# Kernel optimization log

Measured on AMD Instinct MI355X. Metric: run time of the kernel, lower is better.

Reference implementation:

```python
import jax, jax.numpy as jnp
import numpy as np

# PEPS grid configuration (matches init_kwargs)
X, Y = 4, 4            # xnodes, ynodes
D = 6                  # bond_dim
P = 2                  # features_in (physical dim)
F = 10                 # features_out (forced by result.view([10]))
CX, CY = X // 2, Y // 2  # center node carries the output leg
BATCH = 2048


def node_labels(i, j):
    # bond labels after the physical index is contracted away; axis order: up, left, down, right, out
    labs = []
    if i > 0: labs.append(f'v{i-1}_{j}')   # up bond (shared with row i-1)
    if j > 0: labs.append(f'h{i}_{j-1}')   # left bond (shared with col j-1)
    if i < X - 1: labs.append(f'v{i}_{j}') # down bond
    if j < Y - 1: labs.append(f'h{i}_{j}') # right bond
    if (i, j) == (CX, CY): labs.append('o')  # output leg on center node
    return labs


def node_shape(i, j):
    shp = [P]  # physical axis first (input_nodes[i][j][0] ^ peps_nodes[i][j][0])
    shp += [D] * (int(i > 0) + int(j > 0) + int(i < X - 1) + int(j < Y - 1))
    if (i, j) == (CX, CY): shp.append(F)
    return tuple(shp)


def setup_inputs() -> dict:
    key = jax.random.key(0)
    keys = jax.random.split(key, X * Y + 1)
    inp = {"x": jax.random.normal(keys[0], (BATCH, X, Y, P), dtype=jnp.float32)}
    k = 1
    for i in range(X):
        for j in range(Y):
            # simple_peps uniform init with std=0.01
            inp[f"w{i}{j}"] = jax.random.uniform(keys[k], node_shape(i, j), dtype=jnp.float32, minval=-0.01, maxval=0.01)
            k += 1
    return inp


def _td(a, alabs, b, blabs):
    """Label-tracked tensordot over all shared bond labels."""
    shared = [l for l in alabs if l in blabs]
    ai = [alabs.index(l) for l in shared]
    bi = [blabs.index(l) for l in shared]
    out = jnp.tensordot(a, b, axes=(ai, bi))
    labs = [l for l in alabs if l not in shared] + [l for l in blabs if l not in shared]
    return out, labs


def _contract_sample(xs, ws):
    # xs: [X, Y, P] one sample; ws: list-of-lists of node tensors
    # 1) contract each input vector into its PEPS node over the physical axis,
    #    then L2-normalize each contracted node (as in func())
    nodes = []
    for i in range(X):
        row = []
        for j in range(Y):
            t = jnp.tensordot(xs[i, j], ws[i][j], axes=(0, 0))
            t = t / jnp.linalg.norm(t)
            row.append(t)
        nodes.append(row)
    # 2) exact contraction of the 2D network, row-by-row boundary sweep
    cur, labs = nodes[0][0], node_labels(0, 0)
    for j in range(1, Y):
        cur, labs = _td(cur, labs, nodes[0][j], node_labels(0, j))
    for i in range(1, X):
        for j in range(Y):
            cur, labs = _td(cur, labs, nodes[i][j], node_labels(i, j))
    out = cur.reshape(F)  # result.view([10])
    return out / jnp.linalg.norm(out)


def reference(x, w00, w01, w02, w03, w10, w11, w12, w13,
              w20, w21, w22, w23, w30, w31, w32, w33):
    ws = [[w00, w01, w02, w03],
          [w10, w11, w12, w13],
          [w20, w21, w22, w23],
          [w30, w31, w32, w33]]
    return jax.vmap(lambda s: _contract_sample(s, ws))(x)  # [B, F]
```

## Files before the change

### kernel.cpp

```cpp
#include <hip/hip_runtime.h>
#include <math.h>

#define NTHREADS 256

struct PW {
    const float* w[16];
    int perp[16];
};

__global__ __launch_bounds__(NTHREADS) void gram16(PW pw, float* __restrict__ g) {
    const int n = blockIdx.x;
    const float* __restrict__ W = pw.w[n];
    const int m = pw.perp[n];
    float s00 = 0.f, s01 = 0.f, s11 = 0.f;
    for (int e = threadIdx.x; e < m; e += NTHREADS) {
        float a = W[e], b = W[m + e];
        s00 += a * a; s01 += a * b; s11 += b * b;
    }
    for (int off = 32; off > 0; off >>= 1) {
        s00 += __shfl_down(s00, off, 64);
        s01 += __shfl_down(s01, off, 64);
        s11 += __shfl_down(s11, off, 64);
    }
    __shared__ float red[4][3];
    const int lane = threadIdx.x & 63, wv = threadIdx.x >> 6;
    if (lane == 0) { red[wv][0] = s00; red[wv][1] = s01; red[wv][2] = s11; }
    __syncthreads();
    if (threadIdx.x == 0) {
        float t0 = 0.f, t1 = 0.f, t2 = 0.f;
        for (int i = 0; i < 4; i++) { t0 += red[i][0]; t1 += red[i][1]; t2 += red[i][2]; }
        g[n * 3 + 0] = t0; g[n * 3 + 1] = t1; g[n * 3 + 2] = t2;
    }
}

template<int X1, int X2, int Y1, int Y2, int U, int L,
         int AX1, int AX2, int AU, int AL,
         int BU, int BLs, int BY1, int BY2,
         int OX1, int OX2, int OY1, int OY2>
__device__ __forceinline__ void contract(const float* __restrict__ A,
                                         const float* __restrict__ Bm,
                                         float* __restrict__ O, int tid) {
    constexpr int ROWS = X1 * X2 * Y1;
    for (int r = tid; r < ROWS; r += NTHREADS) {
        const int x1 = r / (X2 * Y1);
        const int rm = r - x1 * (X2 * Y1);
        const int x2 = rm / Y1;
        const int y1 = rm - x2 * Y1;
        const float* __restrict__ Ab = A + x1 * AX1 + x2 * AX2;
        const float* __restrict__ Bb = Bm + y1 * BY1;
        float acc[Y2];
#pragma unroll
        for (int t = 0; t < Y2; t++) acc[t] = 0.f;
#pragma unroll
        for (int u = 0; u < U; u++) {
#pragma unroll
            for (int l = 0; l < L; l++) {
                const float a = Ab[u * AU + l * AL];
                const float* __restrict__ Bp = Bb + u * BU + l * BLs;
#pragma unroll
                for (int t = 0; t < Y2; t++) acc[t] += a * Bp[t * BY2];
            }
        }
        float* __restrict__ Ob = O + x1 * OX1 + x2 * OX2 + y1 * OY1;
#pragma unroll
        for (int t = 0; t < Y2; t++) Ob[t * OY2] = acc[t];
    }
}

__device__ __forceinline__ void tmat(float* __restrict__ dst, const float* __restrict__ W,
                                     int m, float al, float be, int tid) {
    for (int e = tid; e < m; e += NTHREADS) dst[e] = al * W[e] + be * W[m + e];
}

__global__ __launch_bounds__(NTHREADS) void peps_main(const float* __restrict__ x, PW pw,
                                                      const float* __restrict__ gram,
                                                      float* __restrict__ out) {
    __shared__ float B1[1296], B2[1296], B3[1296], B4[1296], B5[1296];
    __shared__ float tX[1296], tY[1296];
    __shared__ float cfa[16], cfb[16];
    __shared__ float red[4][10];

    const int tid = threadIdx.x;
    const int s = blockIdx.x;

    if (tid < 16) {
        const float a = x[s * 32 + tid * 2 + 0];
        const float b = x[s * 32 + tid * 2 + 1];
        const float g0 = gram[tid * 3 + 0], g1 = gram[tid * 3 + 1], g2 = gram[tid * 3 + 2];
        const float inv = 1.f / sqrtf(a * a * g0 + 2.f * a * b * g1 + b * b * g2);
        cfa[tid] = a * inv; cfb[tid] = b * inv;
    }
    __syncthreads();

#define SYNC __syncthreads()

    tmat(tX, pw.w[0], 36, cfa[0], cfb[0], tid);
    tmat(tY, pw.w[1], 216, cfa[1], cfb[1], tid);
    SYNC;
    contract<1, 6, 6, 6, 6, 1,   0, 6, 1, 0,   36, 0, 6, 1,   0, 36, 6, 1>(tX, tY, B1, tid);
    SYNC;
    tmat(tX, pw.w[4], 216, cfa[4], cfb[4], tid);
    SYNC;
    contract<1, 36, 6, 6, 6, 1,   0, 1, 36, 0,   36, 0, 6, 1,   0, 36, 6, 1>(B1, tX, B2, tid);
    SYNC;
    tmat(tY, pw.w[5], 1296, cfa[5], cfb[5], tid);
    SYNC;
    contract<6, 6, 6, 6, 6, 6,   36, 6, 216, 1,   216, 36, 6, 1,   216, 36, 6, 1>(B2, tY, B3, tid);
    SYNC;

    tmat(tX, pw.w[2], 216, cfa[2], cfb[2], tid);
    tmat(tY, pw.w[3], 36, cfa[3], cfb[3], tid);
    SYNC;
    contract<1, 36, 1, 6, 6, 1,   0, 6, 1, 0,   6, 0, 0, 1,   0, 6, 0, 1>(tX, tY, B1, tid);
    SYNC;
    tmat(tX, pw.w[7], 216, cfa[7], cfb[7], tid);
    SYNC;
    contract<1, 36, 6, 6, 6, 1,   0, 6, 1, 0,   36, 0, 6, 1,   0, 36, 6, 1>(B1, tX, B2, tid);
    SYNC;
    tmat(tY, pw.w[6], 1296, cfa[6], cfb[6], tid);
    SYNC;
    contract<6, 6, 6, 6, 6, 6,   36, 6, 216, 1,   36, 6, 216, 1,   216, 36, 6, 1>(tY, B2, B4, tid);
    SYNC;
    contract<6, 6, 6, 6, 6, 6,   36, 6, 216, 1,   6, 216, 36, 1,   216, 36, 6, 1>(B3, B4, B1, tid);
    SYNC;

    tmat(tX, pw.w[12], 36, cfa[12], cfb[12], tid);
    tmat(tY, pw.w[8], 216, cfa[8], cfb[8], tid);
    SYNC;
    contract<1, 6, 6, 6, 6, 1,   0, 1, 6, 0,   6, 0, 36, 1,   0, 36, 6, 1>(tX, tY, B2, tid);
    SYNC;
    tmat(tX, pw.w[13], 216, cfa[13], cfb[13], tid);
    SYNC;
    contract<1, 36, 6, 6, 6, 1,   0, 1, 36, 0,   6, 0, 36, 1,   0, 36, 6, 1>(B2, tX, B5, tid);
    SYNC;
    tmat(tY, pw.w[9], 1296, cfa[9], cfb[9], tid);
    SYNC;
    contract<6, 6, 6, 6, 6, 6,   216, 1, 36, 6,   36, 6, 216, 1,   216, 36, 6, 1>(B5, tY, B3, tid);
    SYNC;

    tmat(tX, pw.w[11], 216, cfa[11], cfb[11], tid);
    tmat(tY, pw.w[15], 36, cfa[15], cfb[15], tid);
    SYNC;
    contract<6, 6, 1, 6, 6, 1,   36, 6, 1, 0,   6, 0, 0, 1,   36, 6, 0, 1>(tX, tY, B2, tid);
    SYNC;
    tmat(tX, pw.w[14], 216, cfa[14], cfb[14], tid);
    SYNC;
    contract<6, 6, 6, 6, 6, 1,   36, 6, 1, 0,   1, 0, 36, 6,   216, 1, 6, 36>(B2, tX, B4, tid);
    SYNC;

    contract<6, 6, 6, 6, 6, 6,   6, 1, 216, 36,   216, 6, 36, 1,   216, 36, 6, 1>(B1, B3, B5, tid);
    SYNC;
    contract<6, 6, 6, 6, 6, 6,   216, 1, 36, 6,   216, 36, 6, 1,   216, 36, 6, 1>(B5, B4, B2, tid);
    SYNC;

    {
        const float al = cfa[10], be = cfb[10];
        const float* __restrict__ w0 = pw.w[10];
        const float* __restrict__ w1 = w0 + 12960;
        float part[10];
#pragma unroll
        for (int o = 0; o < 10; o++) part[o] = 0.f;
        for (int e = tid; e < 1296; e += NTHREADS) {
            const float Ev = B2[e];
            const float* __restrict__ p0 = w0 + e * 10;
            const float* __restrict__ p1 = w1 + e * 10;
#pragma unroll
            for (int o = 0; o < 10; o++) part[o] += Ev * (al * p0[o] + be * p1[o]);
        }
#pragma unroll
        for (int o = 0; o < 10; o++)
            for (int off = 32; off > 0; off >>= 1)
                part[o] += __shfl_down(part[o], off, 64);
        const int lane = tid & 63, wv = tid >> 6;
        if (lane == 0) {
#pragma unroll
            for (int o = 0; o < 10; o++) red[wv][o] = part[o];
        }
        __syncthreads();
        if (tid == 0) {
            float r[10];
            float ss = 0.f;
#pragma unroll
            for (int o = 0; o < 10; o++) {
                r[o] = red[0][o] + red[1][o] + red[2][o] + red[3][o];
                ss += r[o] * r[o];
            }
            const float inv = 1.f / sqrtf(ss);
#pragma unroll
            for (int o = 0; o < 10; o++) out[s * 10 + o] = r[o] * inv;
        }
    }
#undef SYNC
}

extern "C" void kernel_launch(void* const* d_in, const int* in_sizes, int n_in,
                              void* d_out, int out_size, void* d_ws, size_t ws_size,
                              hipStream_t stream) {
    PW pw;
    for (int k = 0; k < 16; k++) {
        pw.w[k] = (const float*)d_in[1 + k];
        pw.perp[k] = in_sizes[1 + k] / 2;
    }
    float* gram = (float*)d_ws;
    gram16<<<16, NTHREADS, 0, stream>>>(pw, gram);

    const float* x = (const float*)d_in[0];
    const int B = out_size / 10;
    peps_main<<<B, NTHREADS, 0, stream>>>(x, pw, gram, (float*)d_out);
}
```

Before: 161.3 us.

## Process two samples per block with register-tiled contractions and upfront node prep

```diff
diff --git a/kernel.cpp b/kernel.cpp
--- a/kernel.cpp
+++ b/kernel.cpp
@@ -33,161 +33,159 @@
     }
 }
 
-template<int X1, int X2, int Y1, int Y2, int U, int L,
+constexpr int C1 = 0, C2 = 1296, C3 = 2592, PB = 3888;
+constexpr int T00 = 4104, T01 = 4140, T10 = 4356, T11 = 4572;
+constexpr int T02 = 5868, T03 = 6084, T13 = 6120, T12 = 6336;
+constexpr int T30 = 7632, T20 = 7668, T31 = 7884, T21 = 8100;
+constexpr int T23 = 9396, T33 = 9612, T32 = 9648;
+constexpr int ARENA = 9864;
+
+template<int M, int DST>
+__device__ __forceinline__ void tmat2(float* __restrict__ lds, const float* __restrict__ W,
+                                      float a0, float b0, float a1, float b1, int tid) {
+    for (int e = tid; e < 2 * M; e += NTHREADS) {
+        const int s = (e >= M) ? 1 : 0;
+        const int idx = e - s * M;
+        const float al = s ? a1 : a0;
+        const float be = s ? b1 : b0;
+        lds[s * ARENA + DST + idx] = al * W[idx] + be * W[M + idx];
+    }
+}
+
+template<int X1, int X2, int Y1, int Y2, int U, int L, int TX,
          int AX1, int AX2, int AU, int AL,
-         int BU, int BLs, int BY1, int BY2,
-         int OX1, int OX2, int OY1, int OY2>
-__device__ __forceinline__ void contract(const float* __restrict__ A,
-                                         const float* __restrict__ Bm,
-                                         float* __restrict__ O, int tid) {
-    constexpr int ROWS = X1 * X2 * Y1;
-    for (int r = tid; r < ROWS; r += NTHREADS) {
-        const int x1 = r / (X2 * Y1);
-        const int rm = r - x1 * (X2 * Y1);
-        const int x2 = rm / Y1;
-        const int y1 = rm - x2 * Y1;
-        const float* __restrict__ Ab = A + x1 * AX1 + x2 * AX2;
-        const float* __restrict__ Bb = Bm + y1 * BY1;
-        float acc[Y2];
-#pragma unroll
-        for (int t = 0; t < Y2; t++) acc[t] = 0.f;
+         int BU, int BLS, int BY1, int BY2,
+         int OX1, int OX2, int OY1, int OY2,
+         int AOFF, int BOFF, int OOFF>
+__device__ __forceinline__ void step2(float* __restrict__ lds, int tid) {
+    constexpr int XB = X2 / TX;
+    constexpr int TILES = X1 * XB * Y1;
+    constexpr int TOT = 2 * TILES;
+    for (int t = tid; t < TOT; t += NTHREADS) {
+        const int sl = t / TILES;
+        const int r = t - sl * TILES;
+        const int x1 = r / (XB * Y1);
+        const int rm = r - x1 * (XB * Y1);
+        const int xb = rm / Y1;
+        const int y1 = rm - xb * Y1;
+        const float* __restrict__ Ab = lds + sl * ARENA + AOFF + x1 * AX1 + xb * TX * AX2;
+        const float* __restrict__ Bb = lds + sl * ARENA + BOFF + y1 * BY1;
+        float acc[TX][Y2];
+#pragma unroll
+        for (int i = 0; i < TX; i++)
+#pragma unroll
+            for (int t2 = 0; t2 < Y2; t2++) acc[i][t2] = 0.f;
 #pragma unroll
         for (int u = 0; u < U; u++) {
 #pragma unroll
             for (int l = 0; l < L; l++) {
-                const float a = Ab[u * AU + l * AL];
-                const float* __restrict__ Bp = Bb + u * BU + l * BLs;
-#pragma unroll
-                for (int t = 0; t < Y2; t++) acc[t] += a * Bp[t * BY2];
-            }
-        }
-        float* __restrict__ Ob = O + x1 * OX1 + x2 * OX2 + y1 * OY1;
-#pragma unroll
-        for (int t = 0; t < Y2; t++) Ob[t * OY2] = acc[t];
-    }
-}
-
-__device__ __forceinline__ void tmat(float* __restrict__ dst, const float* __restrict__ W,
-                                     int m, float al, float be, int tid) {
-    for (int e = tid; e < m; e += NTHREADS) dst[e] = al * W[e] + be * W[m + e];
+                float a[TX];
+#pragma unroll
+                for (int i = 0; i < TX; i++) a[i] = Ab[i * AX2 + u * AU + l * AL];
+                const float* __restrict__ Bp = Bb + u * BU + l * BLS;
+#pragma unroll
+                for (int t2 = 0; t2 < Y2; t2++) {
+                    const float bv = Bp[t2 * BY2];
+#pragma unroll
+                    for (int i = 0; i < TX; i++) acc[i][t2] += a[i] * bv;
+                }
+            }
+        }
+        float* __restrict__ Ob = lds + sl * ARENA + OOFF + x1 * OX1 + xb * TX * OX2 + y1 * OY1;
+#pragma unroll
+        for (int i = 0; i < TX; i++)
+#pragma unroll
+            for (int t2 = 0; t2 < Y2; t2++) Ob[i * OX2 + t2 * OY2] = acc[i][t2];
+    }
 }
 
 __global__ __launch_bounds__(NTHREADS) void peps_main(const float* __restrict__ x, PW pw,
                                                       const float* __restrict__ gram,
                                                       float* __restrict__ out) {
-    __shared__ float B1[1296], B2[1296], B3[1296], B4[1296], B5[1296];
-    __shared__ float tX[1296], tY[1296];
-    __shared__ float cfa[16], cfb[16];
-    __shared__ float red[4][10];
+    __shared__ float lds[2 * ARENA];
+    __shared__ float cfa[2][16], cfb[2][16];
+    __shared__ float red[4][2][10];
 
     const int tid = threadIdx.x;
-    const int s = blockIdx.x;
-
-    if (tid < 16) {
-        const float a = x[s * 32 + tid * 2 + 0];
-        const float b = x[s * 32 + tid * 2 + 1];
-        const float g0 = gram[tid * 3 + 0], g1 = gram[tid * 3 + 1], g2 = gram[tid * 3 + 2];
+    const int s0 = blockIdx.x * 2;
+
+    if (tid < 32) {
+        const int sl = tid >> 4, n = tid & 15;
+        const float a = x[(s0 + sl) * 32 + n * 2 + 0];
+        const float b = x[(s0 + sl) * 32 + n * 2 + 1];
+        const float g0 = gram[n * 3 + 0], g1 = gram[n * 3 + 1], g2 = gram[n * 3 + 2];
         const float inv = 1.f / sqrtf(a * a * g0 + 2.f * a * b * g1 + b * b * g2);
-        cfa[tid] = a * inv; cfb[tid] = b * inv;
+        cfa[sl][n] = a * inv; cfb[sl][n] = b * inv;
     }
     __syncthreads();
 
+#define TM(M, DST, WI) tmat2<M, DST>(lds, pw.w[WI], cfa[0][WI], cfb[0][WI], cfa[1][WI], cfb[1][WI], tid)
+    TM(36, T00, 0);  TM(216, T01, 1);  TM(216, T10, 4);  TM(1296, T11, 5);
+    TM(216, T02, 2); TM(36, T03, 3);   TM(216, T13, 7);  TM(1296, T12, 6);
+    TM(36, T30, 12); TM(216, T20, 8);  TM(216, T31, 13); TM(1296, T21, 9);
+    TM(216, T23, 11); TM(36, T33, 15); TM(216, T32, 14);
+#undef TM
+    __syncthreads();
+
 #define SYNC __syncthreads()
-
-    tmat(tX, pw.w[0], 36, cfa[0], cfb[0], tid);
-    tmat(tY, pw.w[1], 216, cfa[1], cfb[1], tid);
-    SYNC;
-    contract<1, 6, 6, 6, 6, 1,   0, 6, 1, 0,   36, 0, 6, 1,   0, 36, 6, 1>(tX, tY, B1, tid);
-    SYNC;
-    tmat(tX, pw.w[4], 216, cfa[4], cfb[4], tid);
-    SYNC;
-    contract<1, 36, 6, 6, 6, 1,   0, 1, 36, 0,   36, 0, 6, 1,   0, 36, 6, 1>(B1, tX, B2, tid);
-    SYNC;
-    tmat(tY, pw.w[5], 1296, cfa[5], cfb[5], tid);
-    SYNC;
-    contract<6, 6, 6, 6, 6, 6,   36, 6, 216, 1,   216, 36, 6, 1,   216, 36, 6, 1>(B2, tY, B3, tid);
-    SYNC;
-
-    tmat(tX, pw.w[2], 216, cfa[2], cfb[2], tid);
-    tmat(tY, pw.w[3], 36, cfa[3], cfb[3], tid);
-    SYNC;
-    contract<1, 36, 1, 6, 6, 1,   0, 6, 1, 0,   6, 0, 0, 1,   0, 6, 0, 1>(tX, tY, B1, tid);
-    SYNC;
-    tmat(tX, pw.w[7], 216, cfa[7], cfb[7], tid);
-    SYNC;
-    contract<1, 36, 6, 6, 6, 1,   0, 6, 1, 0,   36, 0, 6, 1,   0, 36, 6, 1>(B1, tX, B2, tid);
-    SYNC;
-    tmat(tY, pw.w[6], 1296, cfa[6], cfb[6], tid);
-    SYNC;
-    contract<6, 6, 6, 6, 6, 6,   36, 6, 216, 1,   36, 6, 216, 1,   216, 36, 6, 1>(tY, B2, B4, tid);
-    SYNC;
-    contract<6, 6, 6, 6, 6, 6,   36, 6, 216, 1,   6, 216, 36, 1,   216, 36, 6, 1>(B3, B4, B1, tid);
-    SYNC;
-
-    tmat(tX, pw.w[12], 36, cfa[12], cfb[12], tid);
-    tmat(tY, pw.w[8], 216, cfa[8], cfb[8], tid);
-    SYNC;
-    contract<1, 6, 6, 6, 6, 1,   0, 1, 6, 0,   6, 0, 36, 1,   0, 36, 6, 1>(tX, tY, B2, tid);
-    SYNC;
-    tmat(tX, pw.w[13], 216, cfa[13], cfb[13], tid);
-    SYNC;
-    contract<1, 36, 6, 6, 6, 1,   0, 1, 36, 0,   6, 0, 36, 1,   0, 36, 6, 1>(B2, tX, B5, tid);
-    SYNC;
-    tmat(tY, pw.w[9], 1296, cfa[9], cfb[9], tid);
-    SYNC;
-    contract<6, 6, 6, 6, 6, 6,   216, 1, 36, 6,   36, 6, 216, 1,   216, 36, 6, 1>(B5, tY, B3, tid);
-    SYNC;
-
-    tmat(tX, pw.w[11], 216, cfa[11], cfb[11], tid);
-    tmat(tY, pw.w[15], 36, cfa[15], cfb[15], tid);
-    SYNC;
-    contract<6, 6, 1, 6, 6, 1,   36, 6, 1, 0,   6, 0, 0, 1,   36, 6, 0, 1>(tX, tY, B2, tid);
-    SYNC;
-    tmat(tX, pw.w[14], 216, cfa[14], cfb[14], tid);
-    SYNC;
-    contract<6, 6, 6, 6, 6, 1,   36, 6, 1, 0,   1, 0, 36, 6,   216, 1, 6, 36>(B2, tX, B4, tid);
-    SYNC;
-
-    contract<6, 6, 6, 6, 6, 6,   6, 1, 216, 36,   216, 6, 36, 1,   216, 36, 6, 1>(B1, B3, B5, tid);
-    SYNC;
-    contract<6, 6, 6, 6, 6, 6,   216, 1, 36, 6,   216, 36, 6, 1,   216, 36, 6, 1>(B5, B4, B2, tid);
-    SYNC;
+    step2<1, 6, 6, 6, 6, 1, 2,  0, 6, 1, 0,   36, 0, 6, 1,   0, 36, 6, 1,  T00, T01, PB>(lds, tid); SYNC;
+    step2<1, 36, 6, 6, 6, 1, 2,  0, 1, 36, 0,  36, 0, 6, 1,   0, 36, 6, 1,  PB, T10, C1>(lds, tid); SYNC;
+    step2<6, 6, 6, 6, 6, 6, 2,  36, 6, 216, 1, 216, 36, 6, 1, 216, 36, 6, 1, C1, T11, C2>(lds, tid); SYNC;
+    step2<1, 36, 1, 6, 6, 1, 2,  0, 6, 1, 0,   6, 0, 0, 1,    0, 6, 0, 1,   T02, T03, PB>(lds, tid); SYNC;
+    step2<1, 36, 6, 6, 6, 1, 2,  0, 6, 1, 0,   36, 0, 6, 1,   0, 36, 6, 1,  PB, T13, C1>(lds, tid); SYNC;
+    step2<6, 6, 6, 6, 6, 6, 2,  36, 6, 216, 1, 36, 6, 216, 1, 216, 36, 6, 1, T12, C1, C3>(lds, tid); SYNC;
+    step2<6, 6, 6, 6, 6, 6, 2,  36, 6, 216, 1, 6, 216, 36, 1, 216, 36, 6, 1, C2, C3, C1>(lds, tid); SYNC;
+    step2<1, 6, 6, 6, 6, 1, 2,  0, 1, 6, 0,    6, 0, 36, 1,   0, 36, 6, 1,  T30, T20, PB>(lds, tid); SYNC;
+    step2<1, 36, 6, 6, 6, 1, 2,  0, 1, 36, 0,  6, 0, 36, 1,   0, 36, 6, 1,  PB, T31, C2>(lds, tid); SYNC;
+    step2<6, 6, 6, 6, 6, 6, 2,  216, 1, 36, 6, 36, 6, 216, 1, 216, 36, 6, 1, C2, T21, C3>(lds, tid); SYNC;
+    step2<6, 6, 6, 6, 6, 6, 2,  6, 1, 216, 36, 216, 6, 36, 1, 216, 36, 6, 1, C1, C3, C2>(lds, tid); SYNC;
+    step2<6, 6, 1, 6, 6, 1, 2,  36, 6, 1, 0,   6, 0, 0, 1,    36, 6, 0, 1,  T23, T33, PB>(lds, tid); SYNC;
+    step2<6, 6, 6, 6, 6, 1, 2,  36, 6, 1, 0,   1, 0, 36, 6,   216, 1, 6, 36, PB, T32, C1>(lds, tid); SYNC;
+    step2<6, 6, 6, 6, 6, 6, 2,  216, 1, 36, 6, 216, 36, 6, 1, 216, 36, 6, 1, C2, C1, C3>(lds, tid); SYNC;
 
     {
-        const float al = cfa[10], be = cfb[10];
+        const float a0 = cfa[0][10], b0 = cfb[0][10];
+        const float a1 = cfa[1][10], b1 = cfb[1][10];
         const float* __restrict__ w0 = pw.w[10];
         const float* __restrict__ w1 = w0 + 12960;
-        float part[10];
-#pragma unroll
-        for (int o = 0; o < 10; o++) part[o] = 0.f;
+        float p0[10], p1[10];
+#pragma unroll
+        for (int o = 0; o < 10; o++) { p0[o] = 0.f; p1[o] = 0.f; }
         for (int e = tid; e < 1296; e += NTHREADS) {
-            const float Ev = B2[e];
-            const float* __restrict__ p0 = w0 + e * 10;
-            const float* __restrict__ p1 = w1 + e * 10;
-#pragma unroll
-            for (int o = 0; o < 10; o++) part[o] += Ev * (al * p0[o] + be * p1[o]);
+            const float E0 = lds[C3 + e];
+            const float E1 = lds[ARENA + C3 + e];
+            const float* __restrict__ q0 = w0 + e * 10;
+            const float* __restrict__ q1 = w1 + e * 10;
+#pragma unroll
+            for (int o = 0; o < 10; o++) {
+                const float v0 = q0[o], v1 = q1[o];
+                p0[o] += E0 * (a0 * v0 + b0 * v1);
+                p1[o] += E1 * (a1 * v0 + b1 * v1);
+            }
         }
 #pragma unroll
         for (int o = 0; o < 10; o++)
-            for (int off = 32; off > 0; off >>= 1)
-                part[o] += __shfl_down(part[o], off, 64);
+            for (int off = 32; off > 0; off >>= 1) {
+                p0[o] += __shfl_down(p0[o], off, 64);
+                p1[o] += __shfl_down(p1[o], off, 64);
+            }
         const int lane = tid & 63, wv = tid >> 6;
         if (lane == 0) {
 #pragma unroll
-            for (int o = 0; o < 10; o++) red[wv][o] = part[o];
+            for (int o = 0; o < 10; o++) { red[wv][0][o] = p0[o]; red[wv][1][o] = p1[o]; }
         }
         __syncthreads();
-        if (tid == 0) {
+        if (tid < 2) {
             float r[10];
             float ss = 0.f;
 #pragma unroll
             for (int o = 0; o < 10; o++) {
-                r[o] = red[0][o] + red[1][o] + red[2][o] + red[3][o];
+                r[o] = red[0][tid][o] + red[1][tid][o] + red[2][tid][o] + red[3][tid][o];
                 ss += r[o] * r[o];
             }
             const float inv = 1.f / sqrtf(ss);
 #pragma unroll
-            for (int o = 0; o < 10; o++) out[s * 10 + o] = r[o] * inv;
+            for (int o = 0; o < 10; o++) out[(s0 + tid) * 10 + o] = r[o] * inv;
         }
     }
 #undef SYNC
@@ -206,5 +204,5 @@
 
     const float* x = (const float*)d_in[0];
     const int B = out_size / 10;
-    peps_main<<<B, NTHREADS, 0, stream>>>(x, pw, gram, (float*)d_out);
-}
+    peps_main<<<B / 2, NTHREADS, 0, stream>>>(x, pw, gram, (float*)d_out);
+}
```

New measurement: 157.8 us. -2.2%, faster.
